# Kernel tuning notes

Hardware: AMD Instinct MI355X
Metric: run time of the kernel (lower is better)

Reference implementation:

```python
import jax, jax.numpy as jnp
import numpy as np

EPS = 1e-5
QMAX = 127.0

def activation_quant(x):
    # per-token (last-dim) abs-max int8 fake-quant
    x_max = jnp.clip(jnp.max(jnp.abs(x), axis=-1, keepdims=True), EPS, None)
    scale = QMAX / x_max
    q = jnp.clip(jnp.round(x * scale), -128.0, 127.0)
    return q / scale

def setup_inputs() -> dict:
    key = jax.random.key(0)
    kx, kw = jax.random.split(key)
    x = jax.random.normal(kx, (4, 8192, 2048), dtype=jnp.float32)
    # ternary {-1, 0, 1} weight, stored int8 in torch, cast to float for the GEMM
    W = jax.random.randint(kw, (2048, 2048), -1, 2).astype(jnp.float32)  # [out, in]
    return {"x": x, "W": W}

def reference(x, W):
    # straight-through estimator form: x + sg(quant(x) - x)
    x_quant = x + jax.lax.stop_gradient(activation_quant(x) - x)
    # y = x_quant @ W.T  (F.linear)
    return jnp.einsum('bsd,od->bso', x_quant, W)
```

## Files before the change

kernel.cpp:

```cpp
#include <hip/hip_runtime.h>

typedef int v4i __attribute__((ext_vector_type(4)));

#define KDIM 2048
#define NDIM 2048

#define GLOAD16(g, l) __builtin_amdgcn_global_load_lds(                      \
    (const __attribute__((address_space(1))) void*)(g),                      \
    (__attribute__((address_space(3))) void*)(l), 16, 0, 0)


__device__ __forceinline__ int pack4q(float4 v, float s) {
  int a = __float2int_rn(v.x * s);
  int b = __float2int_rn(v.y * s);
  int c = __float2int_rn(v.z * s);
  int d = __float2int_rn(v.w * s);
  a = max(-128, min(127, a)); b = max(-128, min(127, b));
  c = max(-128, min(127, c)); d = max(-128, min(127, d));
  return (a & 0xff) | ((b & 0xff) << 8) | ((c & 0xff) << 16) | ((d & 0xff) << 24);
}

__global__ __launch_bounds__(256) void quant_rows(const float* __restrict__ x,
                                                  signed char* __restrict__ q,
                                                  float* __restrict__ rscale) {
  const int row = blockIdx.x;
  const float4* xr = (const float4*)(x + (size_t)row * KDIM);
  float4 v0 = xr[threadIdx.x];
  float4 v1 = xr[256 + threadIdx.x];
  float m = fmaxf(fmaxf(fabsf(v0.x), fabsf(v0.y)), fmaxf(fabsf(v0.z), fabsf(v0.w)));
  m = fmaxf(m, fmaxf(fmaxf(fabsf(v1.x), fabsf(v1.y)), fmaxf(fabsf(v1.z), fabsf(v1.w))));
  #pragma unroll
  for (int off = 32; off > 0; off >>= 1) m = fmaxf(m, __shfl_xor(m, off));
  __shared__ float red[4];
  if ((threadIdx.x & 63) == 0) red[threadIdx.x >> 6] = m;
  __syncthreads();
  float xmax = fmaxf(fmaxf(red[0], red[1]), fmaxf(red[2], red[3]));
  xmax = fmaxf(xmax, 1e-5f);
  const float scale = 127.0f / xmax;
  int* qr = (int*)(q + (size_t)row * KDIM);
  qr[threadIdx.x] = pack4q(v0, scale);
  qr[256 + threadIdx.x] = pack4q(v1, scale);
  if (threadIdx.x == 0) rscale[row] = xmax * (1.0f / 127.0f);
}

__global__ __launch_bounds__(256) void quant_w(const float* __restrict__ W,
                                               signed char* __restrict__ Wq) {
  const int i = blockIdx.x * 256 + threadIdx.x;
  float4 v = ((const float4*)W)[i];
  int a = (int)v.x, b = (int)v.y, c = (int)v.z, d = (int)v.w;
  ((int*)Wq)[i] = (a & 0xff) | ((b & 0xff) << 8) | ((c & 0xff) << 16) | ((d & 0xff) << 24);
}


#define VM8 asm volatile("s_waitcnt vmcnt(8)" ::: "memory")
#define VM4 asm volatile("s_waitcnt vmcnt(4)" ::: "memory")
#define VM0 asm volatile("s_waitcnt vmcnt(0)" ::: "memory")
#define VMNONE

#define STAGE_A(U, T)                                                        \
  GLOAD16(sa + (T) * 64, lds + (U) * 32768 + dstw);                          \
  GLOAD16(sa + (T) * 64 + 128 * KDIM, lds + (U) * 32768 + 8192 + dstw);
#define STAGE_B(U, T)                                                        \
  GLOAD16(sb + (T) * 64, lds + (U) * 32768 + 16384 + dstw);                  \
  GLOAD16(sb + (T) * 64 + 128 * KDIM, lds + (U) * 32768 + 24576 + dstw);

#define MF(m, n, a) acc[m][n] = __builtin_amdgcn_mfma_i32_16x16x64_i8((a), bf[n], acc[m][n], 0, 0, 0);

#define KTILE(U, T, DOSTAGE, VMEND)                                          \
  {                                                                          \
              \
    bf[0] = *(const v4i*)(lds + (U) * 32768 + bRd);                          \
    bf[1] = *(const v4i*)(lds + (U) * 32768 + bRd + 1024);                   \
    bf[2] = *(const v4i*)(lds + (U) * 32768 + bRd + 2048);                   \
    bf[3] = *(const v4i*)(lds + (U) * 32768 + bRd + 3072);                   \
    v4i a0 = *(const v4i*)(lds + (U) * 32768 + aRd);                         \
    v4i a1 = *(const v4i*)(lds + (U) * 32768 + aRd + 1024);                  \
    v4i a2 = *(const v4i*)(lds + (U) * 32768 + aRd + 2048);                  \
    v4i a3 = *(const v4i*)(lds + (U) * 32768 + aRd + 3072);                  \
    v4i a4 = *(const v4i*)(lds + (U) * 32768 + aRd + 4096);                  \
    v4i a5 = *(const v4i*)(lds + (U) * 32768 + aRd + 5120);                  \
    v4i a6 = *(const v4i*)(lds + (U) * 32768 + aRd + 6144);                  \
    v4i a7 = *(const v4i*)(lds + (U) * 32768 + aRd + 7168);                  \
    if (DOSTAGE) {                                                           \
      STAGE_A((((U) + 3) & 3), (T) + 3)                                      \
      STAGE_B((((U) + 3) & 3), (T) + 3)                                      \
    }                                                                        \
    __builtin_amdgcn_s_setprio(1);                                           \
    MF(0, 0, a0) MF(0, 1, a0) MF(0, 2, a0) MF(0, 3, a0)                      \
    MF(1, 0, a1) MF(1, 1, a1) MF(1, 2, a1) MF(1, 3, a1)                      \
    MF(2, 0, a2) MF(2, 1, a2) MF(2, 2, a2) MF(2, 3, a2)                      \
    MF(3, 0, a3) MF(3, 1, a3) MF(3, 2, a3) MF(3, 3, a3)                      \
    MF(4, 0, a4) MF(4, 1, a4) MF(4, 2, a4) MF(4, 3, a4)                      \
    MF(5, 0, a5) MF(5, 1, a5) MF(5, 2, a5) MF(5, 3, a5)                      \
    MF(6, 0, a6) MF(6, 1, a6) MF(6, 2, a6) MF(6, 3, a6)                      \
    MF(7, 0, a7) MF(7, 1, a7) MF(7, 2, a7) MF(7, 3, a7)                      \
    __builtin_amdgcn_s_setprio(0);                                           \
    VMEND;                                                                   \
    __builtin_amdgcn_s_barrier();                                            \
  }

__global__ __launch_bounds__(512, 2) void gemm_i8(const signed char* __restrict__ A,
                                                  const signed char* __restrict__ B,
                                                  const float* __restrict__ rscale,
                                                  float* __restrict__ C) {
  __shared__ __align__(16) signed char lds[131072];
  const int bid = blockIdx.x;
  const int lid = (bid & 7) * 128 + (bid >> 3);
  const int bm = lid >> 3;
  const int bn = lid & 7;
  const int tid = threadIdx.x;
  const int wid = tid >> 6;
  const int lane = tid & 63;
  const int wr = wid >> 2, wc = wid & 3;

  const int srow = wid * 16 + (lane >> 2);
  const int scol = (((lane & 3) ^ ((lane >> 3) & 3)) << 4);
  const signed char* sa = A + (size_t)(bm * 256 + srow) * KDIM + scol;
  const signed char* sb = B + (size_t)(bn * 256 + srow) * KDIM + scol;
  const int dstw = wid << 10;

  const int rslot = (((lane >> 4) ^ ((lane >> 1) & 3)) << 4);
  const int aRd = (wr * 128 + (lane & 15)) * 64 + rslot;
  const int bRd = 16384 + (wc * 64 + (lane & 15)) * 64 + rslot;

  v4i acc[8][4] = {};
  v4i bf[4];

  STAGE_A(0, 0) STAGE_B(0, 0)
  STAGE_A(1, 1) STAGE_B(1, 1)
  STAGE_A(2, 2) STAGE_B(2, 2)
  VM8;
  __builtin_amdgcn_s_barrier();

  for (int ti = 0; ti < 7; ++ti) {
    const int t = ti * 4;
    KTILE(0, t + 0, 1, VM8)
    KTILE(1, t + 1, 1, VM8)
    KTILE(2, t + 2, 1, VM8)
    KTILE(3, t + 3, 1, VM8)
  }
  KTILE(0, 28, 1, VM8)
  KTILE(1, 29, 0, VM4)
  KTILE(2, 30, 0, VM0)
  KTILE(3, 31, 0, VMNONE)

  const int col0 = bn * 256 + wc * 64 + (lane & 15);
  const int rbase = bm * 256 + wr * 128 + ((lane >> 4) << 2);
  #pragma unroll
  for (int m = 0; m < 8; ++m) {
    #pragma unroll
    for (int r = 0; r < 4; ++r) {
      const int row = rbase + m * 16 + r;
      const float s = rscale[row];
      float* crow = C + (size_t)row * NDIM + col0;
      #pragma unroll
      for (int n = 0; n < 4; ++n) crow[n * 16] = (float)acc[m][n][r] * s;
    }
  }
}

extern "C" void kernel_launch(void* const* d_in, const int* in_sizes, int n_in,
                              void* d_out, int out_size, void* d_ws, size_t ws_size,
                              hipStream_t stream) {
  const float* x = (const float*)d_in[0];
  const float* W = (const float*)d_in[1];
  float* out = (float*)d_out;
  const int M = in_sizes[0] / KDIM;

  signed char* q = (signed char*)d_ws;
  signed char* Wq = q + (size_t)M * KDIM;
  float* rscale = (float*)(Wq + (size_t)NDIM * KDIM);

  quant_rows<<<M, 256, 0, stream>>>(x, q, rscale);
  quant_w<<<(NDIM * KDIM / 4) / 256, 256, 0, stream>>>(W, Wq);
  gemm_i8<<<(M / 256) * (NDIM / 256), 512, 0, stream>>>(q, Wq, rscale, out);
}
```

Measured before the change: 249.3 us.

## Double-buffer LDS fragment reads in registers to overlap with MFMA

Each k-tile now loads the next tile's A/B fragments from LDS into a second register set before issuing the current tile's MFMAs. The two sets alternate (fX/fY), and sched_barriers pin the ordering so LDS read latency hides behind matrix math. The vmcnt wait is tightened from 8 to 4 so the next LDS stage is resident before the early read, which cuts global-prefetch slack by one tile. The second fragment set adds roughly 96 VGPRs per thread, which risks spills or lower occupancy.

```diff
diff --git a/kernel.cpp b/kernel.cpp
--- a/kernel.cpp
+++ b/kernel.cpp
@@ -52,51 +52,53 @@
 }
 
 
-#define VM8 asm volatile("s_waitcnt vmcnt(8)" ::: "memory")
 #define VM4 asm volatile("s_waitcnt vmcnt(4)" ::: "memory")
 #define VM0 asm volatile("s_waitcnt vmcnt(0)" ::: "memory")
 #define VMNONE
 
-#define STAGE_A(U, T)                                                        \
+#define STAGE_AB(U, T)                                                       \
   GLOAD16(sa + (T) * 64, lds + (U) * 32768 + dstw);                          \
-  GLOAD16(sa + (T) * 64 + 128 * KDIM, lds + (U) * 32768 + 8192 + dstw);
-#define STAGE_B(U, T)                                                        \
+  GLOAD16(sa + (T) * 64 + 128 * KDIM, lds + (U) * 32768 + 8192 + dstw);      \
   GLOAD16(sb + (T) * 64, lds + (U) * 32768 + 16384 + dstw);                  \
   GLOAD16(sb + (T) * 64 + 128 * KDIM, lds + (U) * 32768 + 24576 + dstw);
 
-#define MF(m, n, a) acc[m][n] = __builtin_amdgcn_mfma_i32_16x16x64_i8((a), bf[n], acc[m][n], 0, 0, 0);
+#define DECLSET(P) v4i P##b0, P##b1, P##b2, P##b3,                           \
+                       P##a0, P##a1, P##a2, P##a3, P##a4, P##a5, P##a6, P##a7;
 
-#define KTILE(U, T, DOSTAGE, VMEND)                                          \
+#define READSET(U, P)                                                        \
+  P##b0 = *(const v4i*)(lds + (U) * 32768 + bRd);                            \
+  P##b1 = *(const v4i*)(lds + (U) * 32768 + bRd + 1024);                     \
+  P##b2 = *(const v4i*)(lds + (U) * 32768 + bRd + 2048);                     \
+  P##b3 = *(const v4i*)(lds + (U) * 32768 + bRd + 3072);                     \
+  P##a0 = *(const v4i*)(lds + (U) * 32768 + aRd);                            \
+  P##a1 = *(const v4i*)(lds + (U) * 32768 + aRd + 1024);                     \
+  P##a2 = *(const v4i*)(lds + (U) * 32768 + aRd + 2048);                     \
+  P##a3 = *(const v4i*)(lds + (U) * 32768 + aRd + 3072);                     \
+  P##a4 = *(const v4i*)(lds + (U) * 32768 + aRd + 4096);                     \
+  P##a5 = *(const v4i*)(lds + (U) * 32768 + aRd + 5120);                     \
+  P##a6 = *(const v4i*)(lds + (U) * 32768 + aRd + 6144);                     \
+  P##a7 = *(const v4i*)(lds + (U) * 32768 + aRd + 7168);
+
+#define MF1(m, n, A, BF) acc[m][n] = __builtin_amdgcn_mfma_i32_16x16x64_i8((A), (BF), acc[m][n], 0, 0, 0);
+#define MFROW(m, A, P)                                                       \
+  MF1(m, 0, A, P##b0) MF1(m, 1, A, P##b1) MF1(m, 2, A, P##b2) MF1(m, 3, A, P##b3)
+#define MFSET(P)                                                             \
+  __builtin_amdgcn_s_setprio(1);                                             \
+  MFROW(0, P##a0, P) MFROW(1, P##a1, P) MFROW(2, P##a2, P)                   \
+  MFROW(3, P##a3, P) MFROW(4, P##a4, P) MFROW(5, P##a5, P)                   \
+  MFROW(6, P##a6, P) MFROW(7, P##a7, P)                                      \
+  __builtin_amdgcn_s_setprio(0);
+
+#define KTILE(U, T, CUR, NXT, DOREAD, DOSTAGE, VMEND)                        \
   {                                                                          \
-              \
-    bf[0] = *(const v4i*)(lds + (U) * 32768 + bRd);                          \
-    bf[1] = *(const v4i*)(lds + (U) * 32768 + bRd + 1024);                   \
-    bf[2] = *(const v4i*)(lds + (U) * 32768 + bRd + 2048);                   \
-    bf[3] = *(const v4i*)(lds + (U) * 32768 + bRd + 3072);                   \
-    v4i a0 = *(const v4i*)(lds + (U) * 32768 + aRd);                         \
-    v4i a1 = *(const v4i*)(lds + (U) * 32768 + aRd + 1024);                  \
-    v4i a2 = *(const v4i*)(lds + (U) * 32768 + aRd + 2048);                  \
-    v4i a3 = *(const v4i*)(lds + (U) * 32768 + aRd + 3072);                  \
-    v4i a4 = *(const v4i*)(lds + (U) * 32768 + aRd + 4096);                  \
-    v4i a5 = *(const v4i*)(lds + (U) * 32768 + aRd + 5120);                  \
-    v4i a6 = *(const v4i*)(lds + (U) * 32768 + aRd + 6144);                  \
-    v4i a7 = *(const v4i*)(lds + (U) * 32768 + aRd + 7168);                  \
-    if (DOSTAGE) {                                                           \
-      STAGE_A((((U) + 3) & 3), (T) + 3)                                      \
-      STAGE_B((((U) + 3) & 3), (T) + 3)                                      \
-    }                                                                        \
-    __builtin_amdgcn_s_setprio(1);                                           \
-    MF(0, 0, a0) MF(0, 1, a0) MF(0, 2, a0) MF(0, 3, a0)                      \
-    MF(1, 0, a1) MF(1, 1, a1) MF(1, 2, a1) MF(1, 3, a1)                      \
-    MF(2, 0, a2) MF(2, 1, a2) MF(2, 2, a2) MF(2, 3, a2)                      \
-    MF(3, 0, a3) MF(3, 1, a3) MF(3, 2, a3) MF(3, 3, a3)                      \
-    MF(4, 0, a4) MF(4, 1, a4) MF(4, 2, a4) MF(4, 3, a4)                      \
-    MF(5, 0, a5) MF(5, 1, a5) MF(5, 2, a5) MF(5, 3, a5)                      \
-    MF(6, 0, a6) MF(6, 1, a6) MF(6, 2, a6) MF(6, 3, a6)                      \
-    MF(7, 0, a7) MF(7, 1, a7) MF(7, 2, a7) MF(7, 3, a7)                      \
-    __builtin_amdgcn_s_setprio(0);                                           \
+    if (DOREAD) { READSET((((U) + 1) & 3), NXT) }                            \
+    if (DOSTAGE) { STAGE_AB((((U) + 3) & 3), (T) + 3) }                      \
+    __builtin_amdgcn_sched_barrier(0);    \
+    MFSET(CUR)                                                               \
+    __builtin_amdgcn_sched_barrier(0);                                       \
     VMEND;                                                                   \
     __builtin_amdgcn_s_barrier();                                            \
+    __builtin_amdgcn_sched_barrier(0);           \
   }
 
 __global__ __launch_bounds__(512, 2) void gemm_i8(const signed char* __restrict__ A,
@@ -124,25 +126,27 @@
   const int bRd = 16384 + (wc * 64 + (lane & 15)) * 64 + rslot;
 
   v4i acc[8][4] = {};
-  v4i bf[4];
+  DECLSET(fX) DECLSET(fY)
 
-  STAGE_A(0, 0) STAGE_B(0, 0)
-  STAGE_A(1, 1) STAGE_B(1, 1)
-  STAGE_A(2, 2) STAGE_B(2, 2)
-  VM8;
+  STAGE_AB(0, 0)
+  STAGE_AB(1, 1)
+  STAGE_AB(2, 2)
+  VM4;
   __builtin_amdgcn_s_barrier();
+  __builtin_amdgcn_sched_barrier(0);
+  READSET(0, fX)
 
   for (int ti = 0; ti < 7; ++ti) {
     const int t = ti * 4;
-    KTILE(0, t + 0, 1, VM8)
-    KTILE(1, t + 1, 1, VM8)
-    KTILE(2, t + 2, 1, VM8)
-    KTILE(3, t + 3, 1, VM8)
+    KTILE(0, t + 0, fX, fY, 1, 1, VM4)
+    KTILE(1, t + 1, fY, fX, 1, 1, VM4)
+    KTILE(2, t + 2, fX, fY, 1, 1, VM4)
+    KTILE(3, t + 3, fY, fX, 1, 1, VM4)
   }
-  KTILE(0, 28, 1, VM8)
-  KTILE(1, 29, 0, VM4)
-  KTILE(2, 30, 0, VM0)
-  KTILE(3, 31, 0, VMNONE)
+  KTILE(0, 28, fX, fY, 1, 1, VM4)
+  KTILE(1, 29, fY, fX, 1, 0, VM0)
+  KTILE(2, 30, fX, fY, 1, 0, VMNONE)
+  KTILE(3, 31, fY, fX, 0, 0, VMNONE)
 
   const int col0 = bn * 256 + wc * 64 + (lane & 15);
   const int rbase = bm * 256 + wr * 128 + ((lane >> 4) << 2);
```

Result: faster. 240.4 us (-3.5%).

## Process GEMM k-tiles in pairs with batched LDS reads and restaged buffers

Applied to the files above, without the earlier changes.

The int8 GEMM main loop now handles two k-tiles per step instead of one. It reads both tiles' A and B fragments from LDS up front, synchronises, and then refills the two freed LDS buffers with tiles four ahead before issuing 64 MFMAs. The aim is to halve the number of barriers and waitcnt points per k-step and give the scheduler a long uninterrupted MFMA run, with sched_barriers enforcing that order. In exchange it holds twice as many fragment registers, which risks spills or lower occupancy, and it waits for all LDS reads to finish before any MFMA starts. It also makes a trivial rewrite of the byte packing in quant_w.

```diff
diff --git a/kernel.cpp b/kernel.cpp
--- a/kernel.cpp
+++ b/kernel.cpp
@@ -48,12 +48,11 @@
   const int i = blockIdx.x * 256 + threadIdx.x;
   float4 v = ((const float4*)W)[i];
   int a = (int)v.x, b = (int)v.y, c = (int)v.z, d = (int)v.w;
-  ((int*)Wq)[i] = (a & 0xff) | ((b & 0xff) << 8) | ((c & 0xff) << 16) | ((d & 0xff) << 24);
+  ((int*)Wq)[i] = (a & 0xff) | ((b << 8) & 0xff00) | ((c << 16) & 0xff0000) | (d << 24);
 }
 
 
 #define VM8 asm volatile("s_waitcnt vmcnt(8)" ::: "memory")
-#define VM4 asm volatile("s_waitcnt vmcnt(4)" ::: "memory")
 #define VM0 asm volatile("s_waitcnt vmcnt(0)" ::: "memory")
 #define VMNONE
 
@@ -64,37 +63,44 @@
   GLOAD16(sb + (T) * 64, lds + (U) * 32768 + 16384 + dstw);                  \
   GLOAD16(sb + (T) * 64 + 128 * KDIM, lds + (U) * 32768 + 24576 + dstw);
 
-#define MF(m, n, a) acc[m][n] = __builtin_amdgcn_mfma_i32_16x16x64_i8((a), bf[n], acc[m][n], 0, 0, 0);
+#define READS(U, P)                                                          \
+  v4i P##a0 = *(const v4i*)(lds + (U) * 32768 + aRd);                        \
+  v4i P##a1 = *(const v4i*)(lds + (U) * 32768 + aRd + 1024);                 \
+  v4i P##a2 = *(const v4i*)(lds + (U) * 32768 + aRd + 2048);                 \
+  v4i P##a3 = *(const v4i*)(lds + (U) * 32768 + aRd + 3072);                 \
+  v4i P##a4 = *(const v4i*)(lds + (U) * 32768 + aRd + 4096);                 \
+  v4i P##a5 = *(const v4i*)(lds + (U) * 32768 + aRd + 5120);                 \
+  v4i P##a6 = *(const v4i*)(lds + (U) * 32768 + aRd + 6144);                 \
+  v4i P##a7 = *(const v4i*)(lds + (U) * 32768 + aRd + 7168);                 \
+  v4i P##b0 = *(const v4i*)(lds + (U) * 32768 + bRd);                        \
+  v4i P##b1 = *(const v4i*)(lds + (U) * 32768 + bRd + 1024);                 \
+  v4i P##b2 = *(const v4i*)(lds + (U) * 32768 + bRd + 2048);                 \
+  v4i P##b3 = *(const v4i*)(lds + (U) * 32768 + bRd + 3072);
 
-#define KTILE(U, T, DOSTAGE, VMEND)                                          \
+#define MF1(m, n, A, B) acc[m][n] = __builtin_amdgcn_mfma_i32_16x16x64_i8((A), (B), acc[m][n], 0, 0, 0);
+#define MFROW(m, P) MF1(m, 0, P##a##m, P##b0) MF1(m, 1, P##a##m, P##b1)      \
+                    MF1(m, 2, P##a##m, P##b2) MF1(m, 3, P##a##m, P##b3)
+#define MFT(P) MFROW(0, P) MFROW(1, P) MFROW(2, P) MFROW(3, P)               \
+               MFROW(4, P) MFROW(5, P) MFROW(6, P) MFROW(7, P)
+
+#define KPAIR(U, T, DOSTAGE, VMEND)                                          \
   {                                                                          \
-              \
-    bf[0] = *(const v4i*)(lds + (U) * 32768 + bRd);                          \
-    bf[1] = *(const v4i*)(lds + (U) * 32768 + bRd + 1024);                   \
-    bf[2] = *(const v4i*)(lds + (U) * 32768 + bRd + 2048);                   \
-    bf[3] = *(const v4i*)(lds + (U) * 32768 + bRd + 3072);                   \
-    v4i a0 = *(const v4i*)(lds + (U) * 32768 + aRd);                         \
-    v4i a1 = *(const v4i*)(lds + (U) * 32768 + aRd + 1024);                  \
-    v4i a2 = *(const v4i*)(lds + (U) * 32768 + aRd + 2048);                  \
-    v4i a3 = *(const v4i*)(lds + (U) * 32768 + aRd + 3072);                  \
-    v4i a4 = *(const v4i*)(lds + (U) * 32768 + aRd + 4096);                  \
-    v4i a5 = *(const v4i*)(lds + (U) * 32768 + aRd + 5120);                  \
-    v4i a6 = *(const v4i*)(lds + (U) * 32768 + aRd + 6144);                  \
-    v4i a7 = *(const v4i*)(lds + (U) * 32768 + aRd + 7168);                  \
+    READS((U), fX)                                                           \
+    READS((U) + 1, fY)                                                       \
+    __builtin_amdgcn_sched_barrier(0);                                       \
+    __builtin_amdgcn_s_barrier();                                            \
+    asm volatile("s_waitcnt lgkmcnt(0)" ::: "memory");                       \
+    __builtin_amdgcn_sched_barrier(0);                                       \
     if (DOSTAGE) {                                                           \
-      STAGE_A((((U) + 3) & 3), (T) + 3)                                      \
-      STAGE_B((((U) + 3) & 3), (T) + 3)                                      \
+      STAGE_A((U), (T) + 4) STAGE_B((U), (T) + 4)                            \
+      STAGE_A((U) + 1, (T) + 5) STAGE_B((U) + 1, (T) + 5)                    \
     }                                                                        \
+    __builtin_amdgcn_sched_barrier(0);                                       \
     __builtin_amdgcn_s_setprio(1);                                           \
-    MF(0, 0, a0) MF(0, 1, a0) MF(0, 2, a0) MF(0, 3, a0)                      \
-    MF(1, 0, a1) MF(1, 1, a1) MF(1, 2, a1) MF(1, 3, a1)                      \
-    MF(2, 0, a2) MF(2, 1, a2) MF(2, 2, a2) MF(2, 3, a2)                      \
-    MF(3, 0, a3) MF(3, 1, a3) MF(3, 2, a3) MF(3, 3, a3)                      \
-    MF(4, 0, a4) MF(4, 1, a4) MF(4, 2, a4) MF(4, 3, a4)                      \
-    MF(5, 0, a5) MF(5, 1, a5) MF(5, 2, a5) MF(5, 3, a5)                      \
-    MF(6, 0, a6) MF(6, 1, a6) MF(6, 2, a6) MF(6, 3, a6)                      \
-    MF(7, 0, a7) MF(7, 1, a7) MF(7, 2, a7) MF(7, 3, a7)                      \
+    MFT(fX)                                                                  \
+    MFT(fY)                                                                  \
     __builtin_amdgcn_s_setprio(0);                                           \
+    __builtin_amdgcn_sched_barrier(0);                                       \
     VMEND;                                                                   \
     __builtin_amdgcn_s_barrier();                                            \
   }
@@ -124,25 +130,21 @@
   const int bRd = 16384 + (wc * 64 + (lane & 15)) * 64 + rslot;
 
   v4i acc[8][4] = {};
-  v4i bf[4];
 
   STAGE_A(0, 0) STAGE_B(0, 0)
   STAGE_A(1, 1) STAGE_B(1, 1)
   STAGE_A(2, 2) STAGE_B(2, 2)
+  STAGE_A(3, 3) STAGE_B(3, 3)
   VM8;
   __builtin_amdgcn_s_barrier();
 
-  for (int ti = 0; ti < 7; ++ti) {
-    const int t = ti * 4;
-    KTILE(0, t + 0, 1, VM8)
-    KTILE(1, t + 1, 1, VM8)
-    KTILE(2, t + 2, 1, VM8)
-    KTILE(3, t + 3, 1, VM8)
+  for (int r2 = 0; r2 < 7; ++r2) {
+    const int t = r2 * 4;
+    KPAIR(0, t + 0, 1, VM8)
+    KPAIR(2, t + 2, 1, VM8)
   }
-  KTILE(0, 28, 1, VM8)
-  KTILE(1, 29, 0, VM4)
-  KTILE(2, 30, 0, VM0)
-  KTILE(3, 31, 0, VMNONE)
+  KPAIR(0, 28, 0, VM0)
+  KPAIR(2, 30, 0, VMNONE)
 
   const int col0 = bn * 256 + wc * 64 + (lane & 15);
   const int rbase = bm * 256 + wr * 128 + ((lane >> 4) << 2);
```

After: 256.0 us. 1.03x slower.

## Interleave LDS reads, global loads and MFMAs in four phases per k-tile

Applied to the files above, without the earlier changes.

Splits each k-tile of the int8 GEMM into four phases. Each phase loads a few A/B fragments from LDS, issues one global-to-LDS load for the next stage, then runs a group of MFMAs, with sched barriers, workgroup barriers and lgkmcnt waits between phases. The aim is to spread LDS traffic and global loads across the MFMA stream and lower register pressure, since fragments are loaded incrementally. The cost is many extra s_barrier instructions per tile, which may add synchronisation stalls. It also rewrites the weight byte-packing expression, which has no effect on speed.

```diff
diff --git a/kernel.cpp b/kernel.cpp
--- a/kernel.cpp
+++ b/kernel.cpp
@@ -48,7 +48,7 @@
   const int i = blockIdx.x * 256 + threadIdx.x;
   float4 v = ((const float4*)W)[i];
   int a = (int)v.x, b = (int)v.y, c = (int)v.z, d = (int)v.w;
-  ((int*)Wq)[i] = (a & 0xff) | ((b & 0xff) << 8) | ((c & 0xff) << 16) | ((d & 0xff) << 24);
+  ((int*)Wq)[i] = (a & 0xff) | ((b << 8) & 0xff00) | ((c << 16) & 0xff0000) | (d << 24);
 }
 
 
@@ -57,46 +57,62 @@
 #define VM0 asm volatile("s_waitcnt vmcnt(0)" ::: "memory")
 #define VMNONE
 
-#define STAGE_A(U, T)                                                        \
-  GLOAD16(sa + (T) * 64, lds + (U) * 32768 + dstw);                          \
-  GLOAD16(sa + (T) * 64 + 128 * KDIM, lds + (U) * 32768 + 8192 + dstw);
-#define STAGE_B(U, T)                                                        \
-  GLOAD16(sb + (T) * 64, lds + (U) * 32768 + 16384 + dstw);                  \
-  GLOAD16(sb + (T) * 64 + 128 * KDIM, lds + (U) * 32768 + 24576 + dstw);
-
-#define MF(m, n, a) acc[m][n] = __builtin_amdgcn_mfma_i32_16x16x64_i8((a), bf[n], acc[m][n], 0, 0, 0);
+#define SB __builtin_amdgcn_sched_barrier(0);
+#define BAR __builtin_amdgcn_s_barrier();
+#define LGKM0 asm volatile("s_waitcnt lgkmcnt(0)" ::: "memory");
+
+#define MF(m, n, A, B) acc[m][n] = __builtin_amdgcn_mfma_i32_16x16x64_i8((A), (B), acc[m][n], 0, 0, 0);
 
 #define KTILE(U, T, DOSTAGE, VMEND)                                          \
   {                                                                          \
-              \
-    bf[0] = *(const v4i*)(lds + (U) * 32768 + bRd);                          \
-    bf[1] = *(const v4i*)(lds + (U) * 32768 + bRd + 1024);                   \
-    bf[2] = *(const v4i*)(lds + (U) * 32768 + bRd + 2048);                   \
-    bf[3] = *(const v4i*)(lds + (U) * 32768 + bRd + 3072);                   \
-    v4i a0 = *(const v4i*)(lds + (U) * 32768 + aRd);                         \
-    v4i a1 = *(const v4i*)(lds + (U) * 32768 + aRd + 1024);                  \
-    v4i a2 = *(const v4i*)(lds + (U) * 32768 + aRd + 2048);                  \
-    v4i a3 = *(const v4i*)(lds + (U) * 32768 + aRd + 3072);                  \
-    v4i a4 = *(const v4i*)(lds + (U) * 32768 + aRd + 4096);                  \
-    v4i a5 = *(const v4i*)(lds + (U) * 32768 + aRd + 5120);                  \
-    v4i a6 = *(const v4i*)(lds + (U) * 32768 + aRd + 6144);                  \
-    v4i a7 = *(const v4i*)(lds + (U) * 32768 + aRd + 7168);                  \
-    if (DOSTAGE) {                                                           \
-      STAGE_A((((U) + 3) & 3), (T) + 3)                                      \
-      STAGE_B((((U) + 3) & 3), (T) + 3)                                      \
-    }                                                                        \
-    __builtin_amdgcn_s_setprio(1);                                           \
-    MF(0, 0, a0) MF(0, 1, a0) MF(0, 2, a0) MF(0, 3, a0)                      \
-    MF(1, 0, a1) MF(1, 1, a1) MF(1, 2, a1) MF(1, 3, a1)                      \
-    MF(2, 0, a2) MF(2, 1, a2) MF(2, 2, a2) MF(2, 3, a2)                      \
-    MF(3, 0, a3) MF(3, 1, a3) MF(3, 2, a3) MF(3, 3, a3)                      \
-    MF(4, 0, a4) MF(4, 1, a4) MF(4, 2, a4) MF(4, 3, a4)                      \
-    MF(5, 0, a5) MF(5, 1, a5) MF(5, 2, a5) MF(5, 3, a5)                      \
-    MF(6, 0, a6) MF(6, 1, a6) MF(6, 2, a6) MF(6, 3, a6)                      \
-    MF(7, 0, a7) MF(7, 1, a7) MF(7, 2, a7) MF(7, 3, a7)                      \
-    __builtin_amdgcn_s_setprio(0);                                           \
+    const int UB = (U) * 32768;                                              \
+    const int SBB = (((U) + 3) & 3) * 32768;                                 \
+                                   \
+    v4i a0 = *(const v4i*)(lds + UB + aRd);                                  \
+    v4i a1 = *(const v4i*)(lds + UB + aRd + 1024);                           \
+    v4i b0 = *(const v4i*)(lds + UB + bRd);                                  \
+    v4i b1 = *(const v4i*)(lds + UB + bRd + 1024);                           \
+    if (DOSTAGE) { GLOAD16(sa + ((T) + 3) * 64, lds + SBB + dstw); }         \
+    SB BAR LGKM0 SB                                                          \
+    __builtin_amdgcn_s_setprio(1);                                           \
+    MF(0, 0, a0, b0) MF(0, 1, a0, b1) MF(1, 0, a1, b0) MF(1, 1, a1, b1)      \
+    __builtin_amdgcn_s_setprio(0);                                           \
+    SB BAR                                                                   \
+                                      \
+    v4i a2 = *(const v4i*)(lds + UB + aRd + 2048);                           \
+    v4i a3 = *(const v4i*)(lds + UB + aRd + 3072);                           \
+    v4i b2 = *(const v4i*)(lds + UB + bRd + 2048);                           \
+    if (DOSTAGE) { GLOAD16(sa + ((T) + 3) * 64 + 128 * KDIM, lds + SBB + 8192 + dstw); } \
+    SB BAR LGKM0 SB                                                          \
+    __builtin_amdgcn_s_setprio(1);                                           \
+    MF(2, 0, a2, b0) MF(2, 1, a2, b1) MF(3, 0, a3, b0) MF(3, 1, a3, b1)      \
+    MF(0, 2, a0, b2) MF(1, 2, a1, b2) MF(2, 2, a2, b2) MF(3, 2, a3, b2)      \
+    __builtin_amdgcn_s_setprio(0);                                           \
+    SB BAR                                                                   \
+                                      \
+    v4i a4 = *(const v4i*)(lds + UB + aRd + 4096);                           \
+    v4i a5 = *(const v4i*)(lds + UB + aRd + 5120);                           \
+    v4i b3 = *(const v4i*)(lds + UB + bRd + 3072);                           \
+    if (DOSTAGE) { GLOAD16(sb + ((T) + 3) * 64, lds + SBB + 16384 + dstw); } \
+    SB BAR LGKM0 SB                                                          \
+    __builtin_amdgcn_s_setprio(1);                                           \
+    MF(0, 3, a0, b3) MF(1, 3, a1, b3) MF(2, 3, a2, b3) MF(3, 3, a3, b3)      \
+    MF(4, 0, a4, b0) MF(4, 1, a4, b1) MF(5, 0, a5, b0) MF(5, 1, a5, b1)      \
+    __builtin_amdgcn_s_setprio(0);                                           \
+    SB BAR                                                                   \
+                    \
+    v4i a6 = *(const v4i*)(lds + UB + aRd + 6144);                           \
+    v4i a7 = *(const v4i*)(lds + UB + aRd + 7168);                           \
+    if (DOSTAGE) { GLOAD16(sb + ((T) + 3) * 64 + 128 * KDIM, lds + SBB + 24576 + dstw); } \
+    SB BAR LGKM0 SB                                                          \
+    __builtin_amdgcn_s_setprio(1);                                           \
+    MF(4, 2, a4, b2) MF(4, 3, a4, b3) MF(5, 2, a5, b2) MF(5, 3, a5, b3)      \
+    MF(6, 0, a6, b0) MF(6, 1, a6, b1) MF(6, 2, a6, b2) MF(6, 3, a6, b3)      \
+    MF(7, 0, a7, b0) MF(7, 1, a7, b1) MF(7, 2, a7, b2) MF(7, 3, a7, b3)      \
+    __builtin_amdgcn_s_setprio(0);                                           \
+    SB                                                                       \
     VMEND;                                                                   \
-    __builtin_amdgcn_s_barrier();                                            \
+    BAR                                                                      \
   }
 
 __global__ __launch_bounds__(512, 2) void gemm_i8(const signed char* __restrict__ A,
@@ -124,11 +140,19 @@
   const int bRd = 16384 + (wc * 64 + (lane & 15)) * 64 + rslot;
 
   v4i acc[8][4] = {};
-  v4i bf[4];
-
-  STAGE_A(0, 0) STAGE_B(0, 0)
-  STAGE_A(1, 1) STAGE_B(1, 1)
-  STAGE_A(2, 2) STAGE_B(2, 2)
+
+  GLOAD16(sa, lds + dstw);
+  GLOAD16(sa + 128 * KDIM, lds + 8192 + dstw);
+  GLOAD16(sb, lds + 16384 + dstw);
+  GLOAD16(sb + 128 * KDIM, lds + 24576 + dstw);
+  GLOAD16(sa + 64, lds + 32768 + dstw);
+  GLOAD16(sa + 64 + 128 * KDIM, lds + 32768 + 8192 + dstw);
+  GLOAD16(sb + 64, lds + 32768 + 16384 + dstw);
+  GLOAD16(sb + 64 + 128 * KDIM, lds + 32768 + 24576 + dstw);
+  GLOAD16(sa + 128, lds + 65536 + dstw);
+  GLOAD16(sa + 128 + 128 * KDIM, lds + 65536 + 8192 + dstw);
+  GLOAD16(sb + 128, lds + 65536 + 16384 + dstw);
+  GLOAD16(sb + 128 + 128 * KDIM, lds + 65536 + 24576 + dstw);
   VM8;
   __builtin_amdgcn_s_barrier();
 
```

After: 236.4 us. -5.1%, faster.
